# Optimization experiments

Measured on AMD Instinct MI355X. Metric: run time of the kernel, lower is better.

The kernel has to match this reference:

```python
import jax, jax.numpy as jnp
from jax import lax
import numpy as np

KSIZE = 3
STRIDE = 1
PAD = 1
SOFTMAX_SCALE = 10.0
EPS = 1e-4


def _unfold(x, k, stride, pad):
    # x: [B, C, H, W] -> ([B, L, C, k, k], Ho, Wo)  (matches torch nn.Unfold ordering)
    B, C, H, W = x.shape
    xp = jnp.pad(x, ((0, 0), (0, 0), (pad, pad), (pad, pad)))
    Ho = (H + 2 * pad - k) // stride + 1
    Wo = (W + 2 * pad - k) // stride + 1
    cols = jnp.stack(
        [xp[:, :, i:i + Ho * stride:stride, j:j + Wo * stride:stride]
         for i in range(k) for j in range(k)], axis=2)  # [B, C, k*k, Ho, Wo]
    cols = cols.reshape(B, C, k, k, Ho * Wo)
    return cols.transpose(0, 4, 1, 2, 3), Ho, Wo


def setup_inputs() -> dict:
    key = jax.random.key(0)
    kb, kf, km = jax.random.split(key, 3)
    b = jax.random.normal(kb, (4, 64, 64, 64), dtype=jnp.float32)
    f = jax.random.normal(kf, (4, 64, 64, 64), dtype=jnp.float32)
    mask = jax.random.uniform(km, (4, 1, 256, 256), dtype=jnp.float32)
    return {"b": b, "f": f, "mask": mask}


def reference(b, f, mask):
    B, C, H, W = f.shape
    k = KSIZE
    # background patches: [B, L, C, k, k]
    bp, _, _ = _unfold(b, k, STRIDE, PAD)
    # mask: avg_pool2d(kernel=4, stride=mask_scale) with mask_scale = mask.W // f.W = 4
    mp = mask.reshape(B, 1, H, 4, W, 4).mean(axis=(3, 5))  # [B, 1, H, W]
    m_unf, _, _ = _unfold(mp, k, STRIDE, PAD)  # [B, L, 1, k, k]
    m0 = m_unf[0]  # quirk of original code: first sample's mask patches used for all
    w = bp * m0[None]  # masked background patches [B, L, C, k, k]
    f_masked = f * (1.0 - mp)
    # L2 norm over (C, k, k) per patch
    norm = jnp.sqrt(jnp.sum(w * w, axis=(2, 3, 4), keepdims=True) + EPS)
    wn = w / norm
    # cosine-similarity score: conv2d(f_masked, wn) as a GEMM over unfolded f
    fp, Ho, Wo = _unfold(f_masked, k, STRIDE, PAD)  # [B, Q, C, k, k]
    score = jnp.einsum('bqcij,blcij->blq', fp, wn).reshape(B, -1, Ho, Wo)  # [B, L, Ho, Wo]
    attn = jax.nn.softmax(score * SOFTMAX_SCALE, axis=1)
    offsets = jnp.argmax(score, axis=1)[:, None]  # [B, 1, Ho, Wo]
    # conv_transpose2d(attn, w, padding=1) == conv2d with spatially flipped, channel-swapped kernel
    pad_ct = k - 1 - 1

    def _ct(a, w_i):  # a: [L, Ho, Wo], w_i: [L, C, k, k]
        kern = jnp.flip(w_i, axis=(-2, -1)).transpose(1, 0, 2, 3)  # [C, L, k, k]
        return lax.conv_general_dilated(
            a[None], kern, (1, 1), [(pad_ct, pad_ct), (pad_ct, pad_ct)],
            dimension_numbers=('NCHW', 'OIHW', 'NCHW'))[0]

    y = jax.vmap(_ct)(attn, w)  # [B, C, Ho, Wo]
    return y, offsets
```

## Files before the change

### kernel.cpp

```cpp
#include <hip/hip_runtime.h>
#include <math.h>

typedef unsigned int u32;
typedef unsigned short u16;
typedef unsigned long long u64;
typedef _Float16 h8v __attribute__((ext_vector_type(8)));
typedef float f4v __attribute__((ext_vector_type(4)));

#define B_ 4
#define C_ 64
#define HW 4096
#define L_ 4096
#define D_ 576
#define MW 256
#define SCALE 10.0f
#define EPS 1e-4f
#define TAU 0.015f
#define PAIRCAP 262144

__device__ __forceinline__ u16 f16b(float x) {
  union { _Float16 h; u16 u; } c; c.h = (_Float16)x; return c.u;
}

__device__ __forceinline__ void gld16(const void* g, void* l) {
  __builtin_amdgcn_global_load_lds((const __attribute__((address_space(1))) void*)g,
                                   (__attribute__((address_space(3))) void*)l, 16, 0, 0);
}

__global__ __launch_bounds__(256) void k_mp(const float* __restrict__ mask, float* __restrict__ mp) {
  int idx = blockIdx.x * 256 + threadIdx.x;
  int b = idx >> 12, p = idx & 4095;
  int y = p >> 6, x = p & 63;
  const float* mb = mask + (size_t)b * MW * MW;
  float s = 0.f;
  #pragma unroll
  for (int i = 0; i < 4; ++i)
    #pragma unroll
    for (int j = 0; j < 4; ++j)
      s += mb[(y * 4 + i) * MW + x * 4 + j];
  mp[idx] = s * (1.f / 16.f);
}

__global__ __launch_bounds__(256) void k_pre2(const float* __restrict__ f, const float* __restrict__ mp,
                                              float* __restrict__ m0, float* __restrict__ fm) {
  int blk = blockIdx.x;
  if (blk < 144) {
    int idx = blk * 256 + threadIdx.x;
    int l = idx / 9, t = idx - l * 9;
    int ly = l >> 6, lx = l & 63;
    int i = t / 3, j = t - i * 3;
    int yy = ly + i - 1, xx = lx + j - 1;
    float v = 0.f;
    if ((unsigned)yy < 64u && (unsigned)xx < 64u) v = mp[(yy << 6) + xx];
    m0[idx] = v;
  } else {
    int idx = (blk - 144) * 256 + threadIdx.x;
    int p = idx & 4095;
    int b = idx >> 18;
    fm[idx] = f[idx] * (1.f - mp[(b << 12) + p]);
  }
}

__global__ __launch_bounds__(256) void k_prep(const float* __restrict__ bimg, const float* __restrict__ fmb,
                                              const float* __restrict__ m0,
                                              u16* __restrict__ w_h, u16* __restrict__ fp_h,
                                              u16* __restrict__ wT_h,
                                              double* __restrict__ norme, float* __restrict__ normv,
                                              int* __restrict__ rcount, int* __restrict__ pcount,
                                              u64* __restrict__ rbest) {
  int blk = blockIdx.x;
  if (blk < 9216) {
    int idx = blk * 256 + threadIdx.x;
    int l = idx / D_, d = idx - l * D_;
    int c = d / 9, t = d - c * 9;
    int ly = l >> 6, lx = l & 63;
    int i = t / 3, j = t - i * 3;
    int yy = ly + i - 1, xx = lx + j - 1;
    float v = 0.f;
    if ((unsigned)yy < 64u && (unsigned)xx < 64u)
      v = bimg[(c << 12) + (yy << 6) + xx] * m0[l * 9 + t];
    w_h[idx] = f16b(v);
  } else if (blk < 10240) {
    int l = (blk - 9216) * 4 + (threadIdx.x >> 6);
    int lane = threadIdx.x & 63;
    int ly = l >> 6, lx = l & 63;
    double s = 0.0;
    for (int i = lane; i < D_; i += 64) {
      int c = i / 9, t = i - c * 9;
      int ii = t / 3, jj = t - ii * 3;
      int yy = ly + ii - 1, xx = lx + jj - 1;
      if ((unsigned)yy < 64u && (unsigned)xx < 64u) {
        float wv = bimg[(c << 12) + (yy << 6) + xx] * m0[l * 9 + t];
        s += (double)wv * (double)wv;
      }
    }
    #pragma unroll
    for (int off = 32; off; off >>= 1) s += __shfl_down(s, off);
    if (lane == 0) {
      double n = sqrt(s + (double)EPS);
      norme[l] = n; normv[l] = (float)n;
    }
  } else if (blk < 20480) {
    int idx = (blk - 10240) * 256 + threadIdx.x;
    int d = idx >> 12, l = idx & 4095;
    float v = 0.f;
    if (d < D_) {
      int c = d / 9, t = d - c * 9;
      int ly = l >> 6, lx = l & 63;
      int i = t / 3, j = t - i * 3;
      int yy = ly + i - 1, xx = lx + j - 1;
      if ((unsigned)yy < 64u && (unsigned)xx < 64u)
        v = bimg[(c << 12) + (yy << 6) + xx] * m0[l * 9 + t];
    }
    wT_h[idx] = f16b(v);
  } else if (blk < 29696) {
    int idx = (blk - 20480) * 256 + threadIdx.x;
    int l = idx / D_, d = idx - l * D_;
    int c = d / 9, t = d - c * 9;
    int ly = l >> 6, lx = l & 63;
    int i = t / 3, j = t - i * 3;
    int yy = ly + i - 1, xx = lx + j - 1;
    float v = 0.f;
    if ((unsigned)yy < 64u && (unsigned)xx < 64u)
      v = fmb[(c << 12) + (yy << 6) + xx];
    fp_h[idx] = f16b(v);
  } else {
    int e = (blk - 29696) * 256 + threadIdx.x;
    rbest[e] = 0ull;
    if (e == 0) { *rcount = 0; *pcount = 0; }
  }
}

#define STAGE(buf, k0) do {                                                              \
    int bb = (buf) * 24576;                                                              \
    _Pragma("unroll") for (int i_ = 0; i_ < 4; ++i_) {                                   \
      int s_ = tid + i_ * 256; int r_ = s_ >> 2, ks_ = s_ & 3;                           \
      int kg_ = ks_ ^ ((r_ >> 1) & 3);                                                   \
      gld16(A + (u32)(m0 + r_) * (u32)lda + (u32)((k0) + kg_ * 8),                       \
            (char*)lds + bb + s_ * 16); }                                                \
    _Pragma("unroll") for (int i_ = 0; i_ < 2; ++i_) {                                   \
      int s_ = tid + i_ * 256; int r_ = s_ >> 2, ks_ = s_ & 3;                           \
      int kg_ = ks_ ^ ((r_ >> 1) & 3);                                                   \
      gld16(Bm + (u32)(n0 + r_) * (u32)ldb + (u32)((k0) + kg_ * 8),                      \
            (char*)lds + bb + 16384 + s_ * 16); }                                        \
  } while (0)

template<int DIVN>
__global__ __launch_bounds__(256, 2) void k_mfma(
    const u16* __restrict__ A, const u16* __restrict__ Bm,
    const float* __restrict__ normv, float* __restrict__ Cout,
    int lda, int ldb, int ldc, int Nlim, int kPerZ, int nChunks, int czStride)
{
  __shared__ u32 lds[12288];
  u16* ldsu = (u16*)lds;
  const int tid = threadIdx.x;
  const int lane = tid & 63, wid = tid >> 6;
  const int wrM = wid >> 1, wc = wid & 1;
  const int kq = lane >> 4, li = lane & 15;

  int nwg = gridDim.x * gridDim.y;
  int bid = blockIdx.y * gridDim.x + blockIdx.x;
  int cpx = nwg >> 3;
  int swz = (bid & 7) * cpx + (bid >> 3);
  int bx = swz % gridDim.x, by = swz / gridDim.x;
  const int m0 = by * 256, n0 = bx * 128;
  const int kz = blockIdx.z * kPerZ;

  f4v acc[8][4] = {};

  STAGE(0, kz);
  __syncthreads();

  for (int kc = 0; kc < nChunks; ++kc) {
    int cur = kc & 1;
    if (kc + 1 < nChunks) STAGE(cur ^ 1, kz + (kc + 1) * 32);

    int cb = cur * 12288;
    h8v ah[8];
    #pragma unroll
    for (int mf = 0; mf < 8; ++mf) {
      int r = wrM * 128 + mf * 16 + li;
      int off = r * 32 + (kq ^ ((r >> 1) & 3)) * 8;
      ah[mf] = *(const h8v*)&ldsu[cb + off];
    }
    #pragma unroll
    for (int nf = 0; nf < 4; ++nf) {
      int r = wc * 64 + nf * 16 + li;
      int off = r * 32 + (kq ^ ((r >> 1) & 3)) * 8;
      h8v bh = *(const h8v*)&ldsu[cb + 8192 + off];
      #pragma unroll
      for (int mf = 0; mf < 8; ++mf)
        acc[mf][nf] = __builtin_amdgcn_mfma_f32_16x16x32_f16(ah[mf], bh, acc[mf][nf], 0, 0, 0);
    }
    if (kc + 1 < nChunks) {
      asm volatile("s_waitcnt vmcnt(0)" ::: "memory");
      __builtin_amdgcn_s_barrier();
      __builtin_amdgcn_sched_barrier(0);
    }
  }

  if (DIVN) {
    #pragma unroll
    for (int nf = 0; nf < 4; ++nf) {
      int n = n0 + wc * 64 + nf * 16 + li;
      float invn = 1.0f / normv[n];
      #pragma unroll
      for (int mf = 0; mf < 8; ++mf) {
        int m = m0 + wrM * 128 + mf * 16 + kq * 4;
        #pragma unroll
        for (int rr = 0; rr < 4; ++rr)
          Cout[(u32)(m + rr) * (u32)ldc + n] = acc[mf][nf][rr] * invn;
      }
    }
  } else {
    float* Cf = Cout + (size_t)blockIdx.z * czStride;
    #pragma unroll
    for (int nf = 0; nf < 4; ++nf) {
      int n = n0 + wc * 64 + nf * 16 + li;
      if (n < Nlim) {
        #pragma unroll
        for (int mf = 0; mf < 8; ++mf) {
          int m = m0 + wrM * 128 + mf * 16 + kq * 4;
          #pragma unroll
          for (int rr = 0; rr < 4; ++rr)
            Cf[(u32)(m + rr) * (u32)ldc + n] = acc[mf][nf][rr];
        }
      }
    }
  }
}

__global__ __launch_bounds__(256) void k_softmax(const float* __restrict__ score, u16* __restrict__ attn,
                                                 float* __restrict__ offs,
                                                 int* __restrict__ rlist, int* __restrict__ rcount,
                                                 u32* __restrict__ pairs, int* __restrict__ pcount) {
  int q = blockIdx.x;
  const float* row = score + (size_t)q * L_;
  u16* arow = attn + (size_t)q * L_;
  int tid = threadIdx.x;
  int wid = tid >> 6, lane = tid & 63;
  __shared__ float smax[4]; __shared__ int sidx[4]; __shared__ float smax2[4]; __shared__ float ssum[4];
  __shared__ int sflag;

  float v[16];
  float v1 = -3.4e38f, v2 = -3.4e38f; int i1 = 0;
  #pragma unroll
  for (int i = 0; i < 16; ++i) {
    int idx = tid + i * 256;
    v[i] = row[idx];
    if (v[i] > v1 || (v[i] == v1 && idx < i1)) { v2 = v1; v1 = v[i]; i1 = idx; }
    else if (v[i] > v2) v2 = v[i];
  }
  #pragma unroll
  for (int off = 32; off; off >>= 1) {
    float ov1 = __shfl_down(v1, off);
    int   oi1 = __shfl_down(i1, off);
    float ov2 = __shfl_down(v2, off);
    if (ov1 > v1 || (ov1 == v1 && oi1 < i1)) { v2 = fmaxf(fmaxf(v2, ov2), v1); v1 = ov1; i1 = oi1; }
    else v2 = fmaxf(fmaxf(v2, ov2), ov1);
  }
  if (lane == 0) { smax[wid] = v1; sidx[wid] = i1; smax2[wid] = v2; }
  __syncthreads();
  if (tid == 0) {
    v1 = smax[0]; i1 = sidx[0]; v2 = smax2[0];
    for (int w = 1; w < 4; ++w) {
      if (smax[w] > v1 || (smax[w] == v1 && sidx[w] < i1)) {
        v2 = fmaxf(fmaxf(v2, smax2[w]), v1); v1 = smax[w]; i1 = sidx[w];
      } else v2 = fmaxf(fmaxf(v2, smax2[w]), smax[w]);
    }
    smax[0] = v1; sidx[0] = i1;
    sflag = (v1 - v2 <= TAU) ? 1 : 0;
    if (sflag) {
      int pos = atomicAdd(rcount, 1);
      if (pos < 4096) rlist[pos] = q;
    }
  }
  __syncthreads();
  float vmax = smax[0];

  if (sflag) {
    float thr = vmax - 2.0f * TAU;
    #pragma unroll
    for (int i = 0; i < 16; ++i) {
      if (v[i] >= thr) {
        int pos = atomicAdd(pcount, 1);
        if (pos < PAIRCAP) pairs[pos] = ((u32)q << 12) | (u32)(tid + i * 256);
      }
    }
  }

  float s = 0.f;
  #pragma unroll
  for (int i = 0; i < 16; ++i) { v[i] = expf((v[i] - vmax) * SCALE); s += v[i]; }
  #pragma unroll
  for (int off = 32; off; off >>= 1) s += __shfl_down(s, off);
  if (lane == 0) ssum[wid] = s;
  __syncthreads();
  if (tid == 0) ssum[0] = ssum[0] + ssum[1] + ssum[2] + ssum[3];
  __syncthreads();
  float inv = 1.f / ssum[0];
  #pragma unroll
  for (int i = 0; i < 16; ++i)
    arow[tid + i * 256] = f16b(v[i] * inv);
  if (tid == 0) offs[q] = (float)sidx[0];
}

__global__ __launch_bounds__(256) void k_rpairs(const u32* __restrict__ pairs, const int* __restrict__ pcount,
                                                const float* __restrict__ b0, const float* __restrict__ m0,
                                                const float* __restrict__ fmb, const double* __restrict__ norme,
                                                u64* __restrict__ rbest) {
  int nw = gridDim.x * 4;
  int gw = blockIdx.x * 4 + (threadIdx.x >> 6);
  int lane = threadIdx.x & 63;
  int cnt = *pcount; if (cnt > PAIRCAP) cnt = PAIRCAP;
  for (int e = gw; e < cnt; e += nw) {
    u32 pr = pairs[e];
    int q = pr >> 12, l = pr & 4095;
    int qy = q >> 6, qx = q & 63, ly = l >> 6, lx = l & 63;
    int c = lane;
    double dot = 0.0;
    #pragma unroll
    for (int t = 0; t < 9; ++t) {
      int i = t / 3, j = t - (t / 3) * 3;
      int wy = ly + i - 1, wx = lx + j - 1;
      int fy = qy + i - 1, fx = qx + j - 1;
      float wv = 0.f, fv = 0.f;
      if ((unsigned)wy < 64u && (unsigned)wx < 64u) wv = b0[(c << 12) + (wy << 6) + wx] * m0[l * 9 + t];
      if ((unsigned)fy < 64u && (unsigned)fx < 64u) fv = fmb[(c << 12) + (fy << 6) + fx];
      dot += (double)wv * (double)fv;
    }
    #pragma unroll
    for (int off = 32; off; off >>= 1) dot += __shfl_down(dot, off);
    if (lane == 0) {
      double sc = dot / norme[l];
      u64 bbits = (u64)__double_as_longlong(sc);
      if (bbits >> 63) bbits = ~bbits; else bbits |= 0x8000000000000000ull;
      u64 key = (bbits & ~0xFFFull) | (u64)(4095 - l);
      atomicMax(rbest + q, key);
    }
  }
}

__global__ __launch_bounds__(256) void k_foldfin(const float* __restrict__ Gp, float* __restrict__ yout,
                                                 const int* __restrict__ rlist, const int* __restrict__ rcount,
                                                 const u64* __restrict__ rbest, float* __restrict__ offs) {
  if (blockIdx.x < 1024) {
    int idx = blockIdx.x * 256 + threadIdx.x;
    int c = idx >> 12, p = idx & 4095;
    int yy = p >> 6, xx = p & 63;
    float s = 0.f;
    #pragma unroll
    for (int t = 0; t < 9; ++t) {
      int i = t / 3, j = t - (t / 3) * 3;
      int qy = yy + 1 - i, qx = xx + 1 - j;
      if ((unsigned)qy < 64u && (unsigned)qx < 64u) {
        u32 base = (u32)((qy << 6) + qx) * D_ + c * 9 + t;
        #pragma unroll
        for (int z = 0; z < 4; ++z) s += Gp[(size_t)z * 2359296 + base];
      }
    }
    yout[idx] = s;
  } else {
    int cnt = *rcount; if (cnt > 4096) cnt = 4096;
    int e = (blockIdx.x - 1024) * 256 + threadIdx.x;
    if (e < cnt) {
      int q = rlist[e];
      offs[q] = (float)(4095 - (int)(rbest[q] & 0xFFFull));
    }
  }
}

extern "C" void kernel_launch(void* const* d_in, const int* in_sizes, int n_in,
                              void* d_out, int out_size, void* d_ws, size_t ws_size,
                              hipStream_t stream) {
  const float* b_in = (const float*)d_in[0];
  const float* f_in = (const float*)d_in[1];
  const float* mask = (const float*)d_in[2];
  float* out = (float*)d_out;

  char* ws = (char*)d_ws;
  float*  mp     = (float*)(ws + 0);
  float*  m0buf  = (float*)(ws + 65536);
  float*  fm     = (float*)(ws + 212992);
  float*  normv  = (float*)(ws + 4407296);
  double* norme  = (double*)(ws + 4423680);
  u16*    w_h    = (u16*)(ws + 4456448);
  u16*    fp_h   = (u16*)(ws + 9175040);
  u16*    wT_h   = (u16*)(ws + 13893632);
  u16*    attn   = (u16*)(ws + 19136512);
  float*  scoreF = (float*)(ws + 52690944);
  float*  Gpart  = (float*)(ws + 52690944);
  int*    rcount = (int*)(ws + 119799808);
  int*    pcount = (int*)(ws + 119799812);
  int*    rlist  = (int*)(ws + 119800064);
  u64*    rbest  = (u64*)(ws + 119816448);
  u32*    pairs  = (u32*)(ws + 119849216);

  k_mp<<<64, 256, 0, stream>>>(mask, mp);
  k_pre2<<<4240, 256, 0, stream>>>(f_in, mp, m0buf, fm);

  for (int b = 0; b < B_; ++b) {
    const float* bimg = b_in + (size_t)b * C_ * HW;
    const float* fmb  = fm + (size_t)b * C_ * HW;
    float* offs_b = out + (size_t)B_ * C_ * HW + (size_t)b * HW;

    k_prep<<<29712, 256, 0, stream>>>(bimg, fmb, m0buf, w_h, fp_h, wT_h,
                                      norme, normv, rcount, pcount, rbest);
    k_mfma<1><<<dim3(32, 16, 1), 256, 0, stream>>>(
        fp_h, w_h, normv, scoreF, D_, D_, L_, L_, 0, 18, 0);
    k_softmax<<<4096, 256, 0, stream>>>(scoreF, attn, offs_b, rlist, rcount, pairs, pcount);
    k_mfma<0><<<dim3(5, 16, 4), 256, 0, stream>>>(
        attn, wT_h, nullptr, Gpart, L_, L_, D_, D_, 1024, 32, 2359296);
    k_rpairs<<<512, 256, 0, stream>>>(pairs, pcount, bimg, m0buf, fmb, norme, rbest);
    k_foldfin<<<1040, 256, 0, stream>>>(Gpart, out + (size_t)b * C_ * HW,
                                        rlist, rcount, rbest, offs_b);
  }
}
```

Before: 653.2 us.

## Fuse softmax into score GEMM epilogue with block-local max and rescale

The score GEMM epilogue now normalizes by patch norm, computes per-128-column block max, top-2 and exp-sum, and writes unnormalized fp16 exp values directly, dropping the fp32 score matrix and the separate softmax pass. A small reduction kernel combines block stats into per-row rescale factors, which the second GEMM applies while staging A tiles through registers into LDS. Candidate pairs for exact refinement are recovered from the fp16 exps via log. Prep kernels also write two fp16 values per thread. The trade-off is extra epilogue work, a register-staged A path in the second GEMM instead of direct LDS loads, and fp16 precision loss in candidate selection.

Result: slower. 896.7 us (+37.3%).

```diff
diff --git a/kernel.cpp b/kernel.cpp
--- a/kernel.cpp
+++ b/kernel.cpp
@@ -6,6 +6,7 @@
 typedef unsigned long long u64;
 typedef _Float16 h8v __attribute__((ext_vector_type(8)));
 typedef float f4v __attribute__((ext_vector_type(4)));
+typedef u32 u4v __attribute__((ext_vector_type(4)));
 
 #define B_ 4
 #define C_ 64
@@ -20,6 +21,9 @@
 
 __device__ __forceinline__ u16 f16b(float x) {
   union { _Float16 h; u16 u; } c; c.h = (_Float16)x; return c.u;
+}
+__device__ __forceinline__ float f16f(u16 v) {
+  union { u16 u; _Float16 h; } c; c.u = v; return (float)c.h;
 }
 
 __device__ __forceinline__ void gld16(const void* g, void* l) {
@@ -61,6 +65,20 @@
   }
 }
 
+__device__ __forceinline__ float patch_val(const float* __restrict__ img, const float* __restrict__ m0,
+                                           int l, int d) {
+  int c = d / 9, t = d - c * 9;
+  int ly = l >> 6, lx = l & 63;
+  int i = t / 3, j = t - i * 3;
+  int yy = ly + i - 1, xx = lx + j - 1;
+  float v = 0.f;
+  if ((unsigned)yy < 64u && (unsigned)xx < 64u) {
+    v = img[(c << 12) + (yy << 6) + xx];
+    if (m0) v *= m0[l * 9 + t];
+  }
+  return v;
+}
+
 __global__ __launch_bounds__(256) void k_prep(const float* __restrict__ bimg, const float* __restrict__ fmb,
                                               const float* __restrict__ m0,
                                               u16* __restrict__ w_h, u16* __restrict__ fp_h,
@@ -69,19 +87,15 @@
                                               int* __restrict__ rcount, int* __restrict__ pcount,
                                               u64* __restrict__ rbest) {
   int blk = blockIdx.x;
-  if (blk < 9216) {
-    int idx = blk * 256 + threadIdx.x;
+  if (blk < 4608) {
+    int gid = blk * 256 + threadIdx.x;
+    int idx = gid * 2;
     int l = idx / D_, d = idx - l * D_;
-    int c = d / 9, t = d - c * 9;
-    int ly = l >> 6, lx = l & 63;
-    int i = t / 3, j = t - i * 3;
-    int yy = ly + i - 1, xx = lx + j - 1;
-    float v = 0.f;
-    if ((unsigned)yy < 64u && (unsigned)xx < 64u)
-      v = bimg[(c << 12) + (yy << 6) + xx] * m0[l * 9 + t];
-    w_h[idx] = f16b(v);
-  } else if (blk < 10240) {
-    int l = (blk - 9216) * 4 + (threadIdx.x >> 6);
+    u32 h0 = f16b(patch_val(bimg, m0, l, d));
+    u32 h1 = f16b(patch_val(bimg, m0, l, d + 1));
+    ((u32*)w_h)[gid] = h0 | (h1 << 16);
+  } else if (blk < 5632) {
+    int l = (blk - 4608) * 4 + (threadIdx.x >> 6);
     int lane = threadIdx.x & 63;
     int ly = l >> 6, lx = l & 63;
     double s = 0.0;
@@ -100,56 +114,48 @@
       double n = sqrt(s + (double)EPS);
       norme[l] = n; normv[l] = (float)n;
     }
-  } else if (blk < 20480) {
-    int idx = (blk - 10240) * 256 + threadIdx.x;
+  } else if (blk < 10752) {
+    int gid = (blk - 5632) * 256 + threadIdx.x;
+    int idx = gid * 2;
     int d = idx >> 12, l = idx & 4095;
-    float v = 0.f;
+    float v0 = 0.f, v1 = 0.f;
     if (d < D_) {
-      int c = d / 9, t = d - c * 9;
-      int ly = l >> 6, lx = l & 63;
-      int i = t / 3, j = t - i * 3;
-      int yy = ly + i - 1, xx = lx + j - 1;
-      if ((unsigned)yy < 64u && (unsigned)xx < 64u)
-        v = bimg[(c << 12) + (yy << 6) + xx] * m0[l * 9 + t];
-    }
-    wT_h[idx] = f16b(v);
-  } else if (blk < 29696) {
-    int idx = (blk - 20480) * 256 + threadIdx.x;
+      v0 = patch_val(bimg, m0, l, d);
+      v1 = patch_val(bimg, m0, l + 1, d);
+    }
+    ((u32*)wT_h)[gid] = (u32)f16b(v0) | ((u32)f16b(v1) << 16);
+  } else if (blk < 15360) {
+    int gid = (blk - 10752) * 256 + threadIdx.x;
+    int idx = gid * 2;
     int l = idx / D_, d = idx - l * D_;
-    int c = d / 9, t = d - c * 9;
-    int ly = l >> 6, lx = l & 63;
-    int i = t / 3, j = t - i * 3;
-    int yy = ly + i - 1, xx = lx + j - 1;
-    float v = 0.f;
-    if ((unsigned)yy < 64u && (unsigned)xx < 64u)
-      v = fmb[(c << 12) + (yy << 6) + xx];
-    fp_h[idx] = f16b(v);
+    u32 h0 = f16b(patch_val(fmb, nullptr, l, d));
+    u32 h1 = f16b(patch_val(fmb, nullptr, l, d + 1));
+    ((u32*)fp_h)[gid] = h0 | (h1 << 16);
   } else {
-    int e = (blk - 29696) * 256 + threadIdx.x;
+    int e = (blk - 15360) * 256 + threadIdx.x;
     rbest[e] = 0ull;
     if (e == 0) { *rcount = 0; *pcount = 0; }
   }
 }
 
-#define STAGE(buf, k0) do {                                                              \
+#define STAGE1(buf, k0) do {                                                             \
     int bb = (buf) * 24576;                                                              \
     _Pragma("unroll") for (int i_ = 0; i_ < 4; ++i_) {                                   \
       int s_ = tid + i_ * 256; int r_ = s_ >> 2, ks_ = s_ & 3;                           \
       int kg_ = ks_ ^ ((r_ >> 1) & 3);                                                   \
-      gld16(A + (u32)(m0 + r_) * (u32)lda + (u32)((k0) + kg_ * 8),                       \
+      gld16(A + (u32)(m0 + r_) * 576u + (u32)((k0) + kg_ * 8),                           \
             (char*)lds + bb + s_ * 16); }                                                \
     _Pragma("unroll") for (int i_ = 0; i_ < 2; ++i_) {                                   \
       int s_ = tid + i_ * 256; int r_ = s_ >> 2, ks_ = s_ & 3;                           \
       int kg_ = ks_ ^ ((r_ >> 1) & 3);                                                   \
-      gld16(Bm + (u32)(n0 + r_) * (u32)ldb + (u32)((k0) + kg_ * 8),                      \
+      gld16(Bm + (u32)(n0 + r_) * 576u + (u32)((k0) + kg_ * 8),                          \
             (char*)lds + bb + 16384 + s_ * 16); }                                        \
   } while (0)
 
-template<int DIVN>
-__global__ __launch_bounds__(256, 2) void k_mfma(
-    const u16* __restrict__ A, const u16* __restrict__ Bm,
-    const float* __restrict__ normv, float* __restrict__ Cout,
-    int lda, int ldb, int ldc, int Nlim, int kPerZ, int nChunks, int czStride)
+__global__ __launch_bounds__(256, 2) void k_mfma1(
+    const u16* __restrict__ A, const u16* __restrict__ Bm, const float* __restrict__ normv,
+    u16* __restrict__ P, float* __restrict__ bm1, int* __restrict__ bi1,
+    float* __restrict__ bm2, float* __restrict__ bsum)
 {
   __shared__ u32 lds[12288];
   u16* ldsu = (u16*)lds;
@@ -164,17 +170,15 @@
   int swz = (bid & 7) * cpx + (bid >> 3);
   int bx = swz % gridDim.x, by = swz / gridDim.x;
   const int m0 = by * 256, n0 = bx * 128;
-  const int kz = blockIdx.z * kPerZ;
 
   f4v acc[8][4] = {};
 
-  STAGE(0, kz);
+  STAGE1(0, 0);
   __syncthreads();
 
-  for (int kc = 0; kc < nChunks; ++kc) {
+  for (int kc = 0; kc < 18; ++kc) {
     int cur = kc & 1;
-    if (kc + 1 < nChunks) STAGE(cur ^ 1, kz + (kc + 1) * 32);
-
+    if (kc + 1 < 18) STAGE1(cur ^ 1, (kc + 1) * 32);
     int cb = cur * 12288;
     h8v ah[8];
     #pragma unroll
@@ -192,117 +196,229 @@
       for (int mf = 0; mf < 8; ++mf)
         acc[mf][nf] = __builtin_amdgcn_mfma_f32_16x16x32_f16(ah[mf], bh, acc[mf][nf], 0, 0, 0);
     }
-    if (kc + 1 < nChunks) {
+    if (kc + 1 < 18) {
       asm volatile("s_waitcnt vmcnt(0)" ::: "memory");
       __builtin_amdgcn_s_barrier();
       __builtin_amdgcn_sched_barrier(0);
     }
   }
-
-  if (DIVN) {
+  __syncthreads();
+
+  float* ldsf = (float*)lds;
+  int*   ldsi = (int*)lds;
+
+  float invn4[4];
+  #pragma unroll
+  for (int nf = 0; nf < 4; ++nf) invn4[nf] = 1.0f / normv[n0 + wc * 64 + nf * 16 + li];
+  #pragma unroll
+  for (int mf = 0; mf < 8; ++mf)
+    #pragma unroll
+    for (int nf = 0; nf < 4; ++nf)
+      #pragma unroll
+      for (int rr = 0; rr < 4; ++rr)
+        acc[mf][nf][rr] *= invn4[nf];
+
+  #pragma unroll
+  for (int mf = 0; mf < 8; ++mf)
+    #pragma unroll
+    for (int rr = 0; rr < 4; ++rr) {
+      float m4 = fmaxf(fmaxf(acc[mf][0][rr], acc[mf][1][rr]), fmaxf(acc[mf][2][rr], acc[mf][3][rr]));
+      #pragma unroll
+      for (int d = 1; d < 16; d <<= 1) m4 = fmaxf(m4, __shfl_xor(m4, d));
+      if (li == 0) ldsf[wc * 256 + wrM * 128 + mf * 16 + kq * 4 + rr] = m4;
+    }
+  __syncthreads();
+
+  #pragma unroll
+  for (int mf = 0; mf < 8; ++mf)
+    #pragma unroll
+    for (int rr = 0; rr < 4; ++rr) {
+      int r128 = mf * 16 + kq * 4 + rr;
+      float bm = fmaxf(ldsf[wrM * 128 + r128], ldsf[256 + wrM * 128 + r128]);
+      int m = m0 + wrM * 128 + r128;
+      float sum4 = 0.f, v1 = -3.4e38f, v2 = -3.4e38f; int i1 = 0x7fffffff;
+      #pragma unroll
+      for (int nf = 0; nf < 4; ++nf) {
+        float sv = acc[mf][nf][rr];
+        int n = n0 + wc * 64 + nf * 16 + li;
+        float p = __expf((sv - bm) * SCALE);
+        P[(u32)m * 4096u + (u32)n] = f16b(p);
+        sum4 += p;
+        if (sv > v1 || (sv == v1 && n < i1)) { v2 = v1; v1 = sv; i1 = n; }
+        else v2 = fmaxf(v2, sv);
+      }
+      #pragma unroll
+      for (int d = 1; d < 16; d <<= 1) {
+        sum4 += __shfl_xor(sum4, d);
+        float ov1 = __shfl_xor(v1, d); int oi1 = __shfl_xor(i1, d); float ov2 = __shfl_xor(v2, d);
+        if (ov1 > v1 || (ov1 == v1 && oi1 < i1)) { v2 = fmaxf(v1, ov2); v1 = ov1; i1 = oi1; }
+        else v2 = fmaxf(v2, ov1);
+      }
+      if (li == 0) {
+        int slot = wc * 256 + wrM * 128 + r128;
+        ldsf[512 + slot] = sum4;
+        ldsf[1024 + slot] = v1;
+        ldsf[1536 + slot] = v2;
+        ldsi[2048 + slot] = i1;
+      }
+    }
+  __syncthreads();
+
+  {
+    float sA = ldsf[512 + tid], sB = ldsf[512 + 256 + tid];
+    float v1a = ldsf[1024 + tid], v1b = ldsf[1024 + 256 + tid];
+    float v2a = ldsf[1536 + tid], v2b = ldsf[1536 + 256 + tid];
+    int   i1a = ldsi[2048 + tid], i1b = ldsi[2048 + 256 + tid];
+    float V1, V2; int I1;
+    if (v1b > v1a) { V1 = v1b; I1 = i1b; V2 = fmaxf(v1a, v2b); }
+    else           { V1 = v1a; I1 = i1a; V2 = fmaxf(v2a, v1b); }
+    int q = m0 + tid, j = n0 >> 7;
+    bm1[q * 32 + j] = V1; bi1[q * 32 + j] = I1; bm2[q * 32 + j] = V2;
+    bsum[q * 32 + j] = sA + sB;
+  }
+}
+
+__global__ __launch_bounds__(256) void k_smred(const float* __restrict__ bm1, const int* __restrict__ bi1,
+                                               const float* __restrict__ bm2, const float* __restrict__ bsum,
+                                               float* __restrict__ fac, float* __restrict__ gm,
+                                               float* __restrict__ offs,
+                                               int* __restrict__ rlist, int* __restrict__ rcount) {
+  int q = blockIdx.x * 4 + (threadIdx.x >> 6);
+  int lane = threadIdx.x & 63;
+  if (lane >= 32) return;
+  float mj = bm1[q * 32 + lane];
+  float v1 = mj; int i1 = bi1[q * 32 + lane];
+  float v2 = bm2[q * 32 + lane];
+  #pragma unroll
+  for (int d = 1; d < 32; d <<= 1) {
+    float ov1 = __shfl_xor(v1, d); int oi1 = __shfl_xor(i1, d); float ov2 = __shfl_xor(v2, d);
+    if (ov1 > v1 || (ov1 == v1 && oi1 < i1)) { v2 = fmaxf(v1, ov2); v1 = ov1; i1 = oi1; }
+    else v2 = fmaxf(v2, ov1);
+  }
+  float e = __expf((mj - v1) * SCALE);
+  float zt = bsum[q * 32 + lane] * e;
+  float Z = zt;
+  #pragma unroll
+  for (int d = 1; d < 32; d <<= 1) Z += __shfl_xor(Z, d);
+  fac[q * 32 + lane] = e / Z;
+  if (lane == 0) {
+    gm[q] = v1;
+    offs[q] = (float)i1;
+    if (v1 - v2 <= TAU) {
+      int pos = atomicAdd(rcount, 1);
+      if (pos < 4096) rlist[pos] = q;
+    }
+  }
+}
+
+__global__ __launch_bounds__(256) void k_cands(const int* __restrict__ rlist, const int* __restrict__ rcount,
+                                               const u16* __restrict__ P, const float* __restrict__ bm1,
+                                               const float* __restrict__ gm,
+                                               u32* __restrict__ pairs, int* __restrict__ pcount) {
+  int cnt = *rcount; if (cnt > 4096) cnt = 4096;
+  for (int e = blockIdx.x; e < cnt; e += gridDim.x) {
+    int q = rlist[e];
+    float thr = gm[q] - 2.0f * TAU - 1e-3f;
+    #pragma unroll
+    for (int i = 0; i < 16; ++i) {
+      int l = threadIdx.x + i * 256;
+      float p = f16f(P[(size_t)q * 4096 + l]);
+      float s = bm1[q * 32 + (l >> 7)] + __logf(p) * (1.0f / SCALE);
+      if (s >= thr) {
+        int pos = atomicAdd(pcount, 1);
+        if (pos < PAIRCAP) pairs[pos] = ((u32)q << 12) | (u32)l;
+      }
+    }
+  }
+}
+
+__global__ __launch_bounds__(256, 2) void k_mfma2(
+    const u16* __restrict__ P, const float* __restrict__ fac, const u16* __restrict__ Bm,
+    float* __restrict__ Gpart)
+{
+  __shared__ u32 lds[12288];
+  u16* ldsu = (u16*)lds;
+  const int tid = threadIdx.x;
+  const int lane = tid & 63, wid = tid >> 6;
+  const int wrM = wid >> 1, wc = wid & 1;
+  const int kq = lane >> 4, li = lane & 15;
+
+  int nwg = gridDim.x * gridDim.y;
+  int bid = blockIdx.y * gridDim.x + blockIdx.x;
+  int cpx = nwg >> 3;
+  int swz = (bid & 7) * cpx + (bid >> 3);
+  int bx = swz % gridDim.x, by = swz / gridDim.x;
+  const int m0 = by * 256, n0 = bx * 128;
+  const int kz = blockIdx.z * 1024;
+
+  f4v acc[8][4] = {};
+  u4v av[4]; float fv[4];
+
+#define ISSUE2(buf, k0) do {                                                             \
+    _Pragma("unroll") for (int i_ = 0; i_ < 4; ++i_) {                                   \
+      int s_ = tid + i_ * 256; int r_ = s_ >> 2, ks_ = s_ & 3;                           \
+      int kg_ = ks_ ^ ((r_ >> 1) & 3);                                                   \
+      int kk_ = (k0) + kg_ * 8;                                                          \
+      av[i_] = *(const u4v*)(P + (size_t)(m0 + r_) * 4096 + kk_);                        \
+      fv[i_] = fac[(m0 + r_) * 32 + (kk_ >> 7)]; }                                       \
+    _Pragma("unroll") for (int i_ = 0; i_ < 2; ++i_) {                                   \
+      int s_ = tid + i_ * 256; int r_ = s_ >> 2, ks_ = s_ & 3;                           \
+      int kg_ = ks_ ^ ((r_ >> 1) & 3);                                                   \
+      gld16(Bm + (u32)(n0 + r_) * 4096u + (u32)((k0) + kg_ * 8),                         \
+            (char*)lds + (buf) * 24576 + 16384 + s_ * 16); }                             \
+  } while (0)
+
+#define WRITE2(buf) do {                                                                 \
+    _Pragma("unroll") for (int i_ = 0; i_ < 4; ++i_) {                                   \
+      int s_ = tid + i_ * 256;                                                           \
+      union { u4v u; h8v h; } cc; cc.u = av[i_];                                         \
+      _Float16 fh = (_Float16)fv[i_];                                                    \
+      cc.h *= (h8v){fh, fh, fh, fh, fh, fh, fh, fh};                                     \
+      *(u4v*)((char*)lds + (buf) * 24576 + s_ * 16) = cc.u; }                            \
+  } while (0)
+
+  ISSUE2(0, kz);
+  WRITE2(0);
+  __syncthreads();
+
+  for (int kc = 0; kc < 32; ++kc) {
+    int cur = kc & 1;
+    if (kc + 1 < 32) ISSUE2(cur ^ 1, kz + (kc + 1) * 32);
+    int cb = cur * 12288;
+    h8v ah[8];
+    #pragma unroll
+    for (int mf = 0; mf < 8; ++mf) {
+      int r = wrM * 128 + mf * 16 + li;
+      int off = r * 32 + (kq ^ ((r >> 1) & 3)) * 8;
+      ah[mf] = *(const h8v*)&ldsu[cb + off];
+    }
     #pragma unroll
     for (int nf = 0; nf < 4; ++nf) {
-      int n = n0 + wc * 64 + nf * 16 + li;
-      float invn = 1.0f / normv[n];
+      int r = wc * 64 + nf * 16 + li;
+      int off = r * 32 + (kq ^ ((r >> 1) & 3)) * 8;
+      h8v bh = *(const h8v*)&ldsu[cb + 8192 + off];
+      #pragma unroll
+      for (int mf = 0; mf < 8; ++mf)
+        acc[mf][nf] = __builtin_amdgcn_mfma_f32_16x16x32_f16(ah[mf], bh, acc[mf][nf], 0, 0, 0);
+    }
+    if (kc + 1 < 32) WRITE2(cur ^ 1);
+    __syncthreads();
+  }
+
+  float* Cf = Gpart + (size_t)blockIdx.z * 2359296;
+  #pragma unroll
+  for (int nf = 0; nf < 4; ++nf) {
+    int n = n0 + wc * 64 + nf * 16 + li;
+    if (n < D_) {
       #pragma unroll
       for (int mf = 0; mf < 8; ++mf) {
         int m = m0 + wrM * 128 + mf * 16 + kq * 4;
         #pragma unroll
         for (int rr = 0; rr < 4; ++rr)
-          Cout[(u32)(m + rr) * (u32)ldc + n] = acc[mf][nf][rr] * invn;
-      }
-    }
-  } else {
-    float* Cf = Cout + (size_t)blockIdx.z * czStride;
-    #pragma unroll
-    for (int nf = 0; nf < 4; ++nf) {
-      int n = n0 + wc * 64 + nf * 16 + li;
-      if (n < Nlim) {
-        #pragma unroll
-        for (int mf = 0; mf < 8; ++mf) {
-          int m = m0 + wrM * 128 + mf * 16 + kq * 4;
-          #pragma unroll
-          for (int rr = 0; rr < 4; ++rr)
-            Cf[(u32)(m + rr) * (u32)ldc + n] = acc[mf][nf][rr];
-        }
-      }
-    }
-  }
-}
-
-__global__ __launch_bounds__(256) void k_softmax(const float* __restrict__ score, u16* __restrict__ attn,
-                                                 float* __restrict__ offs,
-                                                 int* __restrict__ rlist, int* __restrict__ rcount,
-                                                 u32* __restrict__ pairs, int* __restrict__ pcount) {
-  int q = blockIdx.x;
-  const float* row = score + (size_t)q * L_;
-  u16* arow = attn + (size_t)q * L_;
-  int tid = threadIdx.x;
-  int wid = tid >> 6, lane = tid & 63;
-  __shared__ float smax[4]; __shared__ int sidx[4]; __shared__ float smax2[4]; __shared__ float ssum[4];
-  __shared__ int sflag;
-
-  float v[16];
-  float v1 = -3.4e38f, v2 = -3.4e38f; int i1 = 0;
-  #pragma unroll
-  for (int i = 0; i < 16; ++i) {
-    int idx = tid + i * 256;
-    v[i] = row[idx];
-    if (v[i] > v1 || (v[i] == v1 && idx < i1)) { v2 = v1; v1 = v[i]; i1 = idx; }
-    else if (v[i] > v2) v2 = v[i];
-  }
-  #pragma unroll
-  for (int off = 32; off; off >>= 1) {
-    float ov1 = __shfl_down(v1, off);
-    int   oi1 = __shfl_down(i1, off);
-    float ov2 = __shfl_down(v2, off);
-    if (ov1 > v1 || (ov1 == v1 && oi1 < i1)) { v2 = fmaxf(fmaxf(v2, ov2), v1); v1 = ov1; i1 = oi1; }
-    else v2 = fmaxf(fmaxf(v2, ov2), ov1);
-  }
-  if (lane == 0) { smax[wid] = v1; sidx[wid] = i1; smax2[wid] = v2; }
-  __syncthreads();
-  if (tid == 0) {
-    v1 = smax[0]; i1 = sidx[0]; v2 = smax2[0];
-    for (int w = 1; w < 4; ++w) {
-      if (smax[w] > v1 || (smax[w] == v1 && sidx[w] < i1)) {
-        v2 = fmaxf(fmaxf(v2, smax2[w]), v1); v1 = smax[w]; i1 = sidx[w];
-      } else v2 = fmaxf(fmaxf(v2, smax2[w]), smax[w]);
-    }
-    smax[0] = v1; sidx[0] = i1;
-    sflag = (v1 - v2 <= TAU) ? 1 : 0;
-    if (sflag) {
-      int pos = atomicAdd(rcount, 1);
-      if (pos < 4096) rlist[pos] = q;
-    }
-  }
-  __syncthreads();
-  float vmax = smax[0];
-
-  if (sflag) {
-    float thr = vmax - 2.0f * TAU;
-    #pragma unroll
-    for (int i = 0; i < 16; ++i) {
-      if (v[i] >= thr) {
-        int pos = atomicAdd(pcount, 1);
-        if (pos < PAIRCAP) pairs[pos] = ((u32)q << 12) | (u32)(tid + i * 256);
-      }
-    }
-  }
-
-  float s = 0.f;
-  #pragma unroll
-  for (int i = 0; i < 16; ++i) { v[i] = expf((v[i] - vmax) * SCALE); s += v[i]; }
-  #pragma unroll
-  for (int off = 32; off; off >>= 1) s += __shfl_down(s, off);
-  if (lane == 0) ssum[wid] = s;
-  __syncthreads();
-  if (tid == 0) ssum[0] = ssum[0] + ssum[1] + ssum[2] + ssum[3];
-  __syncthreads();
-  float inv = 1.f / ssum[0];
-  #pragma unroll
-  for (int i = 0; i < 16; ++i)
-    arow[tid + i * 256] = f16b(v[i] * inv);
-  if (tid == 0) offs[q] = (float)sidx[0];
+          Cf[(u32)(m + rr) * (u32)D_ + n] = acc[mf][nf][rr];
+      }
+    }
+  }
 }
 
 __global__ __launch_bounds__(256) void k_rpairs(const u32* __restrict__ pairs, const int* __restrict__ pcount,
@@ -387,14 +503,19 @@
   u16*    w_h    = (u16*)(ws + 4456448);
   u16*    fp_h   = (u16*)(ws + 9175040);
   u16*    wT_h   = (u16*)(ws + 13893632);
-  u16*    attn   = (u16*)(ws + 19136512);
-  float*  scoreF = (float*)(ws + 52690944);
-  float*  Gpart  = (float*)(ws + 52690944);
-  int*    rcount = (int*)(ws + 119799808);
-  int*    pcount = (int*)(ws + 119799812);
-  int*    rlist  = (int*)(ws + 119800064);
-  u64*    rbest  = (u64*)(ws + 119816448);
-  u32*    pairs  = (u32*)(ws + 119849216);
+  u16*    P      = (u16*)(ws + 19136512);
+  float*  bm1    = (float*)(ws + 52690944);
+  int*    bi1    = (int*)(ws + 53215232);
+  float*  bm2    = (float*)(ws + 53739520);
+  float*  bsum   = (float*)(ws + 54263808);
+  float*  fac    = (float*)(ws + 54788096);
+  float*  gm     = (float*)(ws + 55312384);
+  float*  Gpart  = (float*)(ws + 55328768);
+  int*    rcount = (int*)(ws + 93077504);
+  int*    pcount = (int*)(ws + 93077508);
+  int*    rlist  = (int*)(ws + 93077760);
+  u64*    rbest  = (u64*)(ws + 93094144);
+  u32*    pairs  = (u32*)(ws + 93126912);
 
   k_mp<<<64, 256, 0, stream>>>(mask, mp);
   k_pre2<<<4240, 256, 0, stream>>>(f_in, mp, m0buf, fm);
@@ -404,13 +525,12 @@
     const float* fmb  = fm + (size_t)b * C_ * HW;
     float* offs_b = out + (size_t)B_ * C_ * HW + (size_t)b * HW;
 
-    k_prep<<<29712, 256, 0, stream>>>(bimg, fmb, m0buf, w_h, fp_h, wT_h,
+    k_prep<<<15376, 256, 0, stream>>>(bimg, fmb, m0buf, w_h, fp_h, wT_h,
                                       norme, normv, rcount, pcount, rbest);
-    k_mfma<1><<<dim3(32, 16, 1), 256, 0, stream>>>(
-        fp_h, w_h, normv, scoreF, D_, D_, L_, L_, 0, 18, 0);
-    k_softmax<<<4096, 256, 0, stream>>>(scoreF, attn, offs_b, rlist, rcount, pairs, pcount);
-    k_mfma<0><<<dim3(5, 16, 4), 256, 0, stream>>>(
-        attn, wT_h, nullptr, Gpart, L_, L_, D_, D_, 1024, 32, 2359296);
+    k_mfma1<<<dim3(32, 16), 256, 0, stream>>>(fp_h, w_h, normv, P, bm1, bi1, bm2, bsum);
+    k_smred<<<1024, 256, 0, stream>>>(bm1, bi1, bm2, bsum, fac, gm, offs_b, rlist, rcount);
+    k_mfma2<<<dim3(5, 16, 4), 256, 0, stream>>>(P, fac, wT_h, Gpart);
+    k_cands<<<64, 256, 0, stream>>>(rlist, rcount, P, bm1, gm, pairs, pcount);
     k_rpairs<<<512, 256, 0, stream>>>(pairs, pcount, bimg, m0buf, fmb, norme, rbest);
     k_foldfin<<<1040, 256, 0, stream>>>(Gpart, out + (size_t)b * C_ * HW,
                                         rlist, rcount, rbest, offs_b);
```
